# Performance work log

Hardware: AMD Instinct MI355X
Metric: run time of the kernel (lower is better)

The kernel has to match this reference:

```python
import math
import jax, jax.numpy as jnp
import numpy as np

NUM_HEADS = 16
NUM_LANDMARKS = 64
INV_ITERS = 6
ATT_SIZE = 1024
HEAD_SIZE = ATT_SIZE // NUM_HEADS  # dk = 64
NEG = -100000.0


def moore_penrose_pinv(x, num_iter):
    # lucidrains-style iterative Moore-Penrose pseudo-inverse
    abs_x = jnp.abs(x)
    col = abs_x.sum(axis=-1)
    row = abs_x.sum(axis=-2)
    z = jnp.swapaxes(x, -1, -2) / (jnp.max(col) * jnp.max(row))
    I = jnp.eye(x.shape[-1], dtype=x.dtype)
    for _ in range(num_iter):
        xz = x @ z
        z = 0.25 * z @ (13.0 * I - xz @ (15.0 * I - xz @ (7.0 * I - xz)))
    return z


def masked_softmax_scores(k, q, mask):
    # q @ k^T (dk=1: q already scaled) + mask, softmax over last dim
    s = jnp.einsum('bhmd,bhld->bhml', q, k)
    if mask is not None:
        s = s + (1.0 - mask) * NEG
    return jax.nn.softmax(s, axis=-1)


def setup_inputs() -> dict:
    key = jax.random.key(0)
    k1, k2, k3 = jax.random.split(key, 3)
    B, L, D = 4, 4096, 1024
    x = jax.random.normal(k1, (B, L, D), dtype=jnp.float32)
    attention_mask = jnp.ones((B, L), dtype=jnp.float32)
    w_kqv = jax.random.normal(k2, (3 * ATT_SIZE, D), dtype=jnp.float32) * 0.02
    w_out = jax.random.normal(k3, (ATT_SIZE, ATT_SIZE), dtype=jnp.float32) * 0.02
    b_out = jnp.zeros((ATT_SIZE,), dtype=jnp.float32)
    return {"x": x, "attention_mask": attention_mask,
            "w_kqv": w_kqv, "w_out": w_out, "b_out": b_out}


def reference(x, attention_mask, w_kqv, w_out, b_out):
    B, L, D = x.shape
    H, nl, hd = NUM_HEADS, NUM_LANDMARKS, HEAD_SIZE
    seg = L // nl  # landmark segment length (L already a multiple of nl)

    kqv = x @ w_kqv.T  # [B, L, 3A]
    k, q, v = jnp.split(kqv, 3, axis=-1)
    split = lambda t: t.reshape(B, L, H, hd).transpose(0, 2, 1, 3)  # [B,H,L,hd]
    k, q, v = split(k), split(q), split(v)

    mask = attention_mask[:, None, :]  # [B,1,L]
    denom = mask.reshape(B, 1, nl, seg).sum(-1) + 1e-08  # [B,1,nl]
    mask_lm = (denom > 0).astype(x.dtype)  # [B,1,nl]
    denom4 = denom[..., None]              # [B,1,nl,1]
    maskL = mask[..., None]                # [B,1,L,1]

    q = q * maskL
    k = k * maskL
    v = v * maskL

    s1_mask = maskL * mask_lm[..., None, :]               # [B,1,L,nl]
    s2_mask = mask_lm[..., None] * mask_lm[..., None, :]  # [B,1,nl,nl]
    s3_mask = jnp.swapaxes(s1_mask, -1, -2)               # [B,1,nl,L]

    q = q / math.sqrt(HEAD_SIZE)
    q_lm = q.reshape(B, H, nl, seg, hd).sum(-2) / denom4  # [B,H,nl,hd]
    k_lm = k.reshape(B, H, nl, seg, hd).sum(-2) / denom4

    scores_1 = masked_softmax_scores(k_lm, q, s1_mask)     # [B,H,L,nl]
    scores_2 = masked_softmax_scores(k_lm, q_lm, s2_mask)  # [B,H,nl,nl]
    scores_3 = masked_softmax_scores(k, q_lm, s3_mask)     # [B,H,nl,L]

    z_star = moore_penrose_pinv(scores_2, INV_ITERS)       # [B,H,nl,nl]
    out = scores_1 @ (z_star @ (scores_3 @ v))             # [B,H,L,hd]

    out = out.transpose(0, 2, 1, 3).reshape(B, L, H * hd)  # merge heads
    return out @ w_out.T + b_out
```

## Files before the change

### kernel.cpp

```cpp
#include <hip/hip_runtime.h>
#include <hip/hip_bf16.h>


static constexpr int Bn  = 4;
static constexpr int Ln  = 4096;
static constexpr int Dn  = 1024;
static constexpr int Hn  = 16;
static constexpr int HDn = 64;
static constexpr int NLn = 64;
static constexpr int SEGn = 64;
static constexpr int BHn = Bn * Hn;
static constexpr int Mn  = Bn * Ln;
static constexpr int NCH = 8;
#define NEG_BIG (-100000.0f)

static constexpr size_t OFF_KT  = 0;
static constexpr size_t OFF_QT  = 16777216;
static constexpr size_t OFF_VT  = 33554432;
static constexpr size_t OFF_WOH = 33554432;
static constexpr size_t OFF_WH  = 50331648;
static constexpr size_t OFF_QLM = 50331648;
static constexpr size_t OFF_KLM = 50593792;
static constexpr size_t OFF_S2  = 50855936;
static constexpr size_t OFF_Z   = 51118080;
static constexpr size_t OFF_WM  = 51380224;
static constexpr size_t OFF_PM  = 51642368;
static constexpr size_t OFF_PS  = 51675136;
static constexpr size_t OFF_GM  = 51707904;
static constexpr size_t OFF_XS  = 53477376;
static constexpr size_t OFF_PO  = 53477376;

using bf16x8 = __attribute__((ext_vector_type(8))) short;
using f32x16 = __attribute__((ext_vector_type(16))) float;
using s16x4  = __attribute__((ext_vector_type(4))) short;

__device__ __forceinline__ unsigned short f2bf(float f) {
    unsigned int u = __float_as_uint(f);
    return (unsigned short)((u + 0x7fffu + ((u >> 16) & 1u)) >> 16);
}
__device__ __forceinline__ void cvt8r(const float* fs, bf16x8& hv) {
    #pragma unroll
    for (int e = 0; e < 8; ++e) hv[e] = (short)f2bf(fs[e]);
}
typedef __attribute__((address_space(1))) void gvoid;
typedef __attribute__((address_space(3))) void lvoid;
__device__ __forceinline__ void async16(void* l, const void* g) {
    __builtin_amdgcn_global_load_lds((gvoid*)(size_t)g, (lvoid*)l, 16, 0, 0);
}

__global__ __launch_bounds__(256) void k_pack(
    const float* __restrict__ src, unsigned short* __restrict__ dh, int row0)
{
    __shared__ float Ls[128][33];
    const int rt = blockIdx.x, kt = blockIdx.y;
    const int tid = threadIdx.x;
    #pragma unroll
    for (int p = 0; p < 4; ++p) {
        const int row = p * 32 + (tid >> 3);
        const int c4 = (tid & 7) * 4;
        const float4 v = *(const float4*)&src[(size_t)(row0 + rt * 128 + row) * 1024 + kt * 32 + c4];
        Ls[row][c4 + 0] = v.x; Ls[row][c4 + 1] = v.y;
        Ls[row][c4 + 2] = v.z; Ls[row][c4 + 3] = v.w;
    }
    __syncthreads();
    const size_t tb = (size_t)(rt * 32 + kt) * 4096;
    for (int s = tid; s < 512; s += 256) {
        const int g = s >> 7, kk = (s >> 6) & 1, l = s & 63;
        const int row = g * 32 + (l & 31);
        const int k0 = kk * 16 + ((l >> 5) & 1) * 8;
        bf16x8 hv;
        cvt8r(&Ls[row][k0], hv);
        *(bf16x8*)&dh[tb + s * 8] = hv;
    }
}

#define GEMM4W_CORE(A_, B_, NNB)                                               \
    __shared__ __attribute__((aligned(16))) char smem[16384];                  \
    const int tid = threadIdx.x;                                               \
    const int lane = tid & 63, wid = tid >> 6;                                 \
    const int cpx = gridDim.x >> 3;                                            \
    const int wg = (blockIdx.x & 7) * cpx + (blockIdx.x >> 3);                 \
    const int bm = wg / (NNB), bn = wg % (NNB);                                \
    const int wrow = wid >> 1, wcol = wid & 1;                                 \
    const unsigned short* gsrc =                                               \
        (wid < 2 ? (A_) + (size_t)bm * 131072 : (B_) + (size_t)bn * 131072)    \
        + (wid & 1) * 2048 + lane * 8;                                         \
    char* ldst = smem + wid * 4096;                                            \
    f32x16 acc[2][2] = {};                                                     \
    for (int kt = 0; kt < 32; ++kt) {                                          \
        const unsigned short* g = gsrc + (size_t)kt * 4096;                    \
        __syncthreads();                                                       \
        _Pragma("unroll")                                                      \
        for (int i = 0; i < 4; ++i)                                            \
            async16(ldst + i * 1024, g + i * 512);                             \
        __syncthreads();                                                       \
        _Pragma("unroll")                                                      \
        for (int kk = 0; kk < 2; ++kk) {                                       \
            bf16x8 fa[2], fb[2];                                               \
            _Pragma("unroll")                                                  \
            for (int ti = 0; ti < 2; ++ti) {                                   \
                const int o = (((wrow * 2 + ti) * 2 + kk) << 10) + lane * 16;  \
                fa[ti] = *(const bf16x8*)(smem + o);                           \
            }                                                                  \
            _Pragma("unroll")                                                  \
            for (int tj = 0; tj < 2; ++tj) {                                   \
                const int o = (((wcol * 2 + tj) * 2 + kk) << 10) + lane * 16;  \
                fb[tj] = *(const bf16x8*)(smem + 8192 + o);                    \
            }                                                                  \
            _Pragma("unroll")                                                  \
            for (int ti = 0; ti < 2; ++ti)                                     \
                _Pragma("unroll")                                              \
                for (int tj = 0; tj < 2; ++tj)                                 \
                    acc[ti][tj] = __builtin_amdgcn_mfma_f32_32x32x16_bf16(     \
                        fa[ti], fb[tj], acc[ti][tj], 0, 0, 0);                 \
        }                                                                      \
    }

__global__ __launch_bounds__(256) void k_kqv_gemm(
    const unsigned short* __restrict__ xh,
    const unsigned short* __restrict__ wh,
    const float* __restrict__ mask,
    float* __restrict__ Kt, float* __restrict__ Qt, float* __restrict__ Vt,
    int row0)
{
    GEMM4W_CORE(xh, wh, 24)
    const int part = bn >> 3;
    #pragma unroll
    for (int ti = 0; ti < 2; ++ti) {
        #pragma unroll
        for (int tj = 0; tj < 2; ++tj) {
            const int col = (bn * 128 + wcol * 64 + tj * 32 + (lane & 31)) & 1023;
            const int h = col >> 6, d = col & 63;
            #pragma unroll
            for (int r = 0; r < 16; ++r) {
                const int row = row0 + bm * 128 + wrow * 64 + ti * 32
                              + (r & 3) + 8 * (r >> 2) + 4 * (lane >> 5);
                const int b = row >> 12, l = row & 4095;
                const float mk = mask[b * Ln + l];
                const size_t idx = ((size_t)(b * Hn + h) * Ln + l) * HDn + d;
                const float v = acc[ti][tj][r] * mk;
                if (part == 0)      Kt[idx] = v;
                else if (part == 1) Qt[idx] = v * 0.125f;
                else                Vt[idx] = v;
            }
        }
    }
}

__global__ __launch_bounds__(256) void k_out_gemm(
    const unsigned short* __restrict__ ah_,
    const unsigned short* __restrict__ bh_,
    const float* __restrict__ bias, float* __restrict__ out)
{
    GEMM4W_CORE(ah_, bh_, 8)
    #pragma unroll
    for (int ti = 0; ti < 2; ++ti) {
        #pragma unroll
        for (int tj = 0; tj < 2; ++tj) {
            const int col = bn * 128 + wcol * 64 + tj * 32 + (lane & 31);
            const float bb = bias[col];
            #pragma unroll
            for (int r = 0; r < 16; ++r) {
                const int row = bm * 128 + wrow * 64 + ti * 32
                              + (r & 3) + 8 * (r >> 2) + 4 * (lane >> 5);
                out[(size_t)row * Dn + col] = acc[ti][tj][r] + bb;
            }
        }
    }
}

__global__ __launch_bounds__(64) void k_landmarks(
    const float* __restrict__ Kt, const float* __restrict__ Qt,
    const float* __restrict__ mask,
    float* __restrict__ klm, float* __restrict__ qlm, int* __restrict__ gmax)
{
    const int blk = blockIdx.x;
    const int m = blk & 63, bh = blk >> 6, b = bh >> 4;
    const int d = threadIdx.x;
    if (blk == 0 && d < 2) gmax[d] = 0;
    float mv = mask[b * Ln + m * SEGn + d];
    #pragma unroll
    for (int off = 32; off; off >>= 1) mv += __shfl_down(mv, off);
    const float denom = __shfl(mv, 0) + 1e-8f;
    const float* kp = Kt + ((size_t)bh * Ln + m * SEGn) * HDn + d;
    const float* qp = Qt + ((size_t)bh * Ln + m * SEGn) * HDn + d;
    float sk = 0.f, sq = 0.f;
    for (int j = 0; j < SEGn; ++j) {
        sk += kp[(size_t)j * HDn];
        sq += qp[(size_t)j * HDn];
    }
    klm[((size_t)bh * NLn + m) * HDn + d] = sk / denom;
    qlm[((size_t)bh * NLn + m) * HDn + d] = sq / denom;
}

__global__ __launch_bounds__(64) void k_s2(
    const float* __restrict__ qlm, const float* __restrict__ klm,
    float* __restrict__ s2, int* __restrict__ gmax)
{
    const int bh = blockIdx.x;
    __shared__ float ql[64][65];
    __shared__ float kl[64][65];
    __shared__ float sr[64][65];
    const int t = threadIdx.x;
    for (int idx = t; idx < 4096; idx += 64) {
        ql[idx >> 6][idx & 63] = qlm[(size_t)bh * 4096 + idx];
        kl[idx >> 6][idx & 63] = klm[(size_t)bh * 4096 + idx];
    }
    __syncthreads();
    float mx = -1e30f;
    for (int mp = 0; mp < 64; ++mp) {
        float s = 0.f;
        #pragma unroll 8
        for (int d2 = 0; d2 < 64; ++d2) s = fmaf(ql[t][d2], kl[mp][d2], s);
        sr[t][mp] = s;
        mx = fmaxf(mx, s);
    }
    float sum = 0.f;
    for (int mp = 0; mp < 64; ++mp) {
        const float e = expf(sr[t][mp] - mx);
        sr[t][mp] = e;
        sum += e;
    }
    const float inv = 1.f / sum;
    float rs = 0.f;
    for (int mp = 0; mp < 64; ++mp) {
        const float v = sr[t][mp] * inv;
        sr[t][mp] = v;
        s2[(size_t)bh * 4096 + t * 64 + mp] = v;
        rs += fabsf(v);
    }
    __syncthreads();
    float cs = 0.f;
    for (int mm = 0; mm < 64; ++mm) cs += fabsf(sr[mm][t]);
    float rmax = rs, cmax = cs;
    #pragma unroll
    for (int off = 32; off; off >>= 1) {
        rmax = fmaxf(rmax, __shfl_down(rmax, off));
        cmax = fmaxf(cmax, __shfl_down(cmax, off));
    }
    if (t == 0) {
        atomicMax(&gmax[0], __float_as_int(rmax));
        atomicMax(&gmax[1], __float_as_int(cmax));
    }
}

template<int SUB>
__device__ __forceinline__ void mm64v(
    float* C, int ldc, const float* Ag, int lda,
    const float* Bm, int ldb, float dg, float scl)
{
    const int tid = threadIdx.x;
    const int tx = tid & 15, ty = tid >> 4;
    const int i0 = ty << 2, j0 = tx << 2;
    float acc[4][4] = {};
    for (int k0 = 0; k0 < 64; k0 += 4) {
        float4 a4[4], b4[4];
        #pragma unroll
        for (int i = 0; i < 4; ++i)
            a4[i] = *(const float4*)&Ag[(size_t)(i0 + i) * lda + k0];
        #pragma unroll
        for (int kk = 0; kk < 4; ++kk)
            b4[kk] = *(const float4*)&Bm[(size_t)(k0 + kk) * ldb + j0];
        if (SUB) {
            #pragma unroll
            for (int kk = 0; kk < 4; ++kk) {
                float* bp = (float*)&b4[kk];
                #pragma unroll
                for (int j = 0; j < 4; ++j)
                    bp[j] = ((k0 + kk == j0 + j) ? dg : 0.0f) - bp[j];
            }
        }
        #pragma unroll
        for (int i = 0; i < 4; ++i) {
            const float* ap = (const float*)&a4[i];
            #pragma unroll
            for (int kk = 0; kk < 4; ++kk) {
                const float* bp = (const float*)&b4[kk];
                #pragma unroll
                for (int j = 0; j < 4; ++j)
                    acc[i][j] = fmaf(ap[kk], bp[j], acc[i][j]);
            }
        }
    }
    __syncthreads();
    #pragma unroll
    for (int i = 0; i < 4; ++i)
        #pragma unroll
        for (int j = 0; j < 4; ++j) C[(size_t)(i0 + i) * ldc + j0 + j] = scl * acc[i][j];
    __syncthreads();
}

__global__ __launch_bounds__(256) void k_pinv(
    const float* __restrict__ s2, const int* __restrict__ gmax,
    float* __restrict__ zout)
{
    __shared__ float Zb[64][68];
    __shared__ float XZ[64][68];
    __shared__ float Tb[64][68];
    const int bh = blockIdx.x;
    const int tid = threadIdx.x;
    const float* X = s2 + (size_t)bh * 4096;
    const float scale = 1.0f / (__int_as_float(gmax[0]) * __int_as_float(gmax[1]));
    for (int idx = tid; idx < 4096; idx += 256) {
        const int i = idx >> 6, j = idx & 63;
        Zb[i][j] = X[j * 64 + i] * scale;
    }
    __syncthreads();
    for (int it = 0; it < 6; ++it) {
        mm64v<0>(&XZ[0][0], 68, X, 64, &Zb[0][0], 68, 0.f, 1.f);
        mm64v<1>(&Tb[0][0], 68, &XZ[0][0], 68, &XZ[0][0], 68, 7.f, 1.f);
        mm64v<1>(&Tb[0][0], 68, &XZ[0][0], 68, &Tb[0][0], 68, 15.f, 1.f);
        mm64v<1>(&Zb[0][0], 68, &Zb[0][0], 68, &Tb[0][0], 68, 13.f, 0.25f);
    }
    for (int idx = tid; idx < 4096; idx += 256)
        zout[(size_t)bh * 4096 + idx] = Zb[idx >> 6][idx & 63];
}

__global__ __launch_bounds__(256) void k_s3v_part(
    const float* __restrict__ qlm, const float* __restrict__ Kt,
    const float* __restrict__ Vt, const float* __restrict__ mask,
    float* __restrict__ Opart, float* __restrict__ mpart, float* __restrict__ spart)
{
    __shared__ float Sm[64][65];
    __shared__ float Ks[64][65];
    __shared__ float Vs[64][65];
    __shared__ unsigned short Qp[4096];
    __shared__ float red[64][4], red2[64][4];
    __shared__ float rowmax[64], rowsum[64], fac[64], mrow[64];
    const int bh = blockIdx.x, ch = blockIdx.y;
    const int b = bh >> 4;
    const int tid = threadIdx.x;
    const int lane = tid & 63, wid = tid >> 6;
    const int wr = wid >> 1, wc = wid & 1;

    for (int idx = tid; idx < 4096; idx += 256)
        Sm[idx >> 6][idx & 63] = qlm[(size_t)bh * 4096 + idx];
    if (tid < 64) { rowmax[tid] = -1e30f; rowsum[tid] = 0.f; }
    __syncthreads();
    for (int s = tid; s < 512; s += 256) {
        const int g = s >> 8, kc = (s >> 6) & 3, l = s & 63;
        const int row = g * 32 + (l & 31);
        const int k0 = kc * 16 + ((l >> 5) & 1) * 8;
        bf16x8 hv;
        cvt8r(&Sm[row][k0], hv);
        *(bf16x8*)&Qp[s * 8] = hv;
    }
    f32x16 accO = {};
    const int t0beg = ch * (Ln / NCH), t0end = t0beg + (Ln / NCH);
    for (int t0 = t0beg; t0 < t0end; t0 += 64) {
        __syncthreads();
        for (int idx = tid; idx < 4096; idx += 256) {
            const int r = idx >> 6, c2 = idx & 63;
            Ks[r][c2] = Kt[((size_t)bh * Ln + t0 + r) * HDn + c2];
            Vs[r][c2] = Vt[((size_t)bh * Ln + t0 + r) * HDn + c2];
        }
        if (tid < 64) mrow[tid] = mask[b * Ln + t0 + tid];
        __syncthreads();
        f32x16 acc = {};
        #pragma unroll
        for (int kc = 0; kc < 4; ++kc) {
            const bf16x8 a_h = *(const bf16x8*)&Qp[((wr * 4 + kc) * 64 + lane) * 8];
            const int brow = wc * 32 + (lane & 31);
            const int k0 = kc * 16 + (lane >> 5) * 8;
            bf16x8 b_h;
            cvt8r(&Ks[brow][k0], b_h);
            acc = __builtin_amdgcn_mfma_f32_32x32x16_bf16(a_h, b_h, acc, 0, 0, 0);
        }
        #pragma unroll
        for (int r = 0; r < 16; ++r) {
            const int row = wr * 32 + (r & 3) + 8 * (r >> 2) + 4 * (lane >> 5);
            const int col = wc * 32 + (lane & 31);
            Sm[row][col] = acc[r] + (1.f - mrow[col]) * NEG_BIG;
        }
        __syncthreads();
        {
            const int row = tid >> 2, sg = tid & 3, c0 = sg * 16;
            float mx = -1e30f;
            #pragma unroll
            for (int c = 0; c < 16; ++c) mx = fmaxf(mx, Sm[row][c0 + c]);
            red[row][sg] = mx;
            __syncthreads();
            const float nm = fmaxf(rowmax[row],
                fmaxf(fmaxf(red[row][0], red[row][1]), fmaxf(red[row][2], red[row][3])));
            const float f = __expf(rowmax[row] - nm);
            float ps = 0.f;
            #pragma unroll
            for (int c = 0; c < 16; ++c) {
                const float e = __expf(Sm[row][c0 + c] - nm);
                Sm[row][c0 + c] = e;
                ps += e;
            }
            red2[row][sg] = ps;
            __syncthreads();
            if (sg == 0) {
                rowsum[row] = rowsum[row] * f
                    + red2[row][0] + red2[row][1] + red2[row][2] + red2[row][3];
                rowmax[row] = nm;
                fac[row] = f;
            }
        }
        __syncthreads();
        #pragma unroll
        for (int r = 0; r < 16; ++r) {
            const int row = wr * 32 + (r & 3) + 8 * (r >> 2) + 4 * (lane >> 5);
            accO[r] *= fac[row];
        }
        #pragma unroll
        for (int kc = 0; kc < 4; ++kc) {
            const int arow = wr * 32 + (lane & 31);
            const int ak0 = kc * 16 + (lane >> 5) * 8;
            bf16x8 a_h;
            cvt8r(&Sm[arow][ak0], a_h);
            const int bcol = wc * 32 + (lane & 31);
            const int bk0 = kc * 16 + (lane >> 5) * 8;
            float bw[8];
            #pragma unroll
            for (int e = 0; e < 8; ++e) bw[e] = Vs[bk0 + e][bcol];
            bf16x8 b_h;
            cvt8r(bw, b_h);
            accO = __builtin_amdgcn_mfma_f32_32x32x16_bf16(a_h, b_h, accO, 0, 0, 0);
        }
    }
    __syncthreads();
    #pragma unroll
    for (int r = 0; r < 16; ++r) {
        const int row = wr * 32 + (r & 3) + 8 * (r >> 2) + 4 * (lane >> 5);
        Vs[row][wc * 32 + (lane & 31)] = accO[r];
    }
    __syncthreads();
    const size_t ob = (size_t)(bh * NCH + ch) * 4096;
    for (int idx = tid; idx < 4096; idx += 256)
        Opart[ob + idx] = Vs[idx >> 6][idx & 63];
    if (tid < 64) {
        mpart[(bh * NCH + ch) * 64 + tid] = rowmax[tid];
        spart[(bh * NCH + ch) * 64 + tid] = rowsum[tid];
    }
}

__global__ __launch_bounds__(256) void k_mergez(
    const float* __restrict__ Opart, const float* __restrict__ mpart,
    const float* __restrict__ spart, const float* __restrict__ Zs,
    float* __restrict__ Wm)
{
    __shared__ float Sv[64][68];
    __shared__ float Zb[64][68];
    const int bh = blockIdx.x, tid = threadIdx.x;
    for (int idx = tid; idx < 4096; idx += 256)
        Zb[idx >> 6][idx & 63] = Zs[(size_t)bh * 4096 + idx];
    {
        const int r = tid >> 2, c0 = (tid & 3) * 16;
        float e[NCH];
        float M = -1e30f;
        #pragma unroll
        for (int c = 0; c < NCH; ++c) {
            e[c] = mpart[(bh * NCH + c) * 64 + r];
            M = fmaxf(M, e[c]);
        }
        float S = 0.f;
        #pragma unroll
        for (int c = 0; c < NCH; ++c) {
            e[c] = expf(e[c] - M);
            S += spart[(bh * NCH + c) * 64 + r] * e[c];
        }
        const float invS = 1.f / S;
        for (int col = c0; col < c0 + 16; ++col) {
            float o = 0.f;
            #pragma unroll
            for (int c = 0; c < NCH; ++c)
                o += Opart[(size_t)(bh * NCH + c) * 4096 + r * 64 + col] * e[c];
            Sv[r][col] = o * invS;
        }
    }
    __syncthreads();
    const int tx = tid & 15, ty = tid >> 4;
    const int i0 = ty << 2, j0 = tx << 2;
    float acc[4][4] = {};
    for (int k0 = 0; k0 < 64; k0 += 4) {
        float4 a4[4], b4[4];
        #pragma unroll
        for (int i = 0; i < 4; ++i)
            a4[i] = *(const float4*)&Zb[i0 + i][k0];
        #pragma unroll
        for (int kk = 0; kk < 4; ++kk)
            b4[kk] = *(const float4*)&Sv[k0 + kk][j0];
        #pragma unroll
        for (int i = 0; i < 4; ++i) {
            const float* ap = (const float*)&a4[i];
            #pragma unroll
            for (int kk = 0; kk < 4; ++kk) {
                const float* bp = (const float*)&b4[kk];
                #pragma unroll
                for (int j = 0; j < 4; ++j)
                    acc[i][j] = fmaf(ap[kk], bp[j], acc[i][j]);
            }
        }
    }
    #pragma unroll
    for (int i = 0; i < 4; ++i)
        #pragma unroll
        for (int j = 0; j < 4; ++j)
            Wm[(size_t)bh * 4096 + (i0 + i) * 64 + j0 + j] = acc[i][j];
}

__global__ __launch_bounds__(256) void k_attn_out(
    const float* __restrict__ Qt, const float* __restrict__ klm,
    const float* __restrict__ Wm, unsigned short* __restrict__ ah)
{
    const int lt = blockIdx.x;
    const int bh = blockIdx.y;
    const int b = bh >> 4, h = bh & 15;
    __shared__ float Sm[64][65];
    __shared__ float Ks[64][65];
    __shared__ float Ws[64][65];
    __shared__ unsigned short Qp[4096];
    __shared__ float red[64][4], red2[64][4];
    __shared__ float invr[64];
    const int tid = threadIdx.x;
    const int lane = tid & 63, wid = tid >> 6;
    const int wr = wid >> 1, wc = wid & 1;

    for (int idx = tid; idx < 4096; idx += 256) {
        const int r = idx >> 6, c2 = idx & 63;
        Sm[r][c2] = Qt[((size_t)bh * Ln + lt * 64 + r) * HDn + c2];
        Ks[r][c2] = klm[(size_t)bh * 4096 + idx];
        Ws[r][c2] = Wm[(size_t)bh * 4096 + idx];
    }
    __syncthreads();
    for (int s = tid; s < 512; s += 256) {
        const int g = s >> 8, kc = (s >> 6) & 3, l = s & 63;
        const int row = g * 32 + (l & 31);
        const int k0 = kc * 16 + ((l >> 5) & 1) * 8;
        bf16x8 hv;
        cvt8r(&Sm[row][k0], hv);
        *(bf16x8*)&Qp[s * 8] = hv;
    }
    __syncthreads();
    f32x16 acc = {};
    #pragma unroll
    for (int kc = 0; kc < 4; ++kc) {
        const bf16x8 a_h = *(const bf16x8*)&Qp[((wr * 4 + kc) * 64 + lane) * 8];
        const int brow = wc * 32 + (lane & 31);
        const int k0 = kc * 16 + (lane >> 5) * 8;
        bf16x8 b_h;
        cvt8r(&Ks[brow][k0], b_h);
        acc = __builtin_amdgcn_mfma_f32_32x32x16_bf16(a_h, b_h, acc, 0, 0, 0);
    }
    #pragma unroll
    for (int r = 0; r < 16; ++r) {
        const int row = wr * 32 + (r & 3) + 8 * (r >> 2) + 4 * (lane >> 5);
        Sm[row][wc * 32 + (lane & 31)] = acc[r];
    }
    __syncthreads();
    {
        const int row = tid >> 2, sg = tid & 3, c0 = sg * 16;
        float mx = -1e30f;
        #pragma unroll
        for (int c = 0; c < 16; ++c) mx = fmaxf(mx, Sm[row][c0 + c]);
        red[row][sg] = mx;
        __syncthreads();
        mx = fmaxf(fmaxf(red[row][0], red[row][1]), fmaxf(red[row][2], red[row][3]));
        float ps = 0.f;
        #pragma unroll
        for (int c = 0; c < 16; ++c) {
            const float e = __expf(Sm[row][c0 + c] - mx);
            Sm[row][c0 + c] = e;
            ps += e;
        }
        red2[row][sg] = ps;
        __syncthreads();
        if (sg == 0)
            invr[row] = 1.f / (red2[row][0] + red2[row][1] + red2[row][2] + red2[row][3]);
    }
    __syncthreads();
    f32x16 acc2 = {};
    #pragma unroll
    for (int kc = 0; kc < 4; ++kc) {
        const int arow = wr * 32 + (lane & 31);
        const int ak0 = kc * 16 + (lane >> 5) * 8;
        bf16x8 a_h;
        cvt8r(&Sm[arow][ak0], a_h);
        const int bcol = wc * 32 + (lane & 31);
        const int bk0 = kc * 16 + (lane >> 5) * 8;
        float bw[8];
        #pragma unroll
        for (int e = 0; e < 8; ++e) bw[e] = Ws[bk0 + e][bcol];
        bf16x8 b_h;
        cvt8r(bw, b_h);
        acc2 = __builtin_amdgcn_mfma_f32_32x32x16_bf16(a_h, b_h, acc2, 0, 0, 0);
    }
    __syncthreads();
    #pragma unroll
    for (int r = 0; r < 16; ++r) {
        const int row = wr * 32 + (r & 3) + 8 * (r >> 2) + 4 * (lane >> 5);
        Ks[row][wc * 32 + (lane & 31)] = acc2[r];
    }
    __syncthreads();
    const int tx = tid & 15, ty = tid >> 4;
    const int i0 = ty << 2, j0 = tx << 2;
    const int kd = h * 64 + j0;
    const int kt2 = kd >> 5, kc2 = kd & 31;
    const int kk2 = kc2 >> 4, half = (kc2 & 15) >> 3, e0 = kc2 & 7;
    #pragma unroll
    for (int i = 0; i < 4; ++i) {
        const float inv = invr[i0 + i];
        const int gm = b * Ln + lt * 64 + i0 + i;
        const int mt = gm >> 7, g2 = (gm & 127) >> 5, lrow = gm & 31;
        const size_t u = (size_t)(mt * 32 + kt2) * 4096
                       + (size_t)(((g2 * 2 + kk2) * 64 + half * 32 + lrow) * 8 + e0);
        s16x4 hv;
        #pragma unroll
        for (int j = 0; j < 4; ++j)
            hv[j] = (short)f2bf(Ks[i0 + i][j0 + j] * inv);
        *(s16x4*)&ah[u] = hv;
    }
}

extern "C" void kernel_launch(void* const* d_in, const int* in_sizes, int n_in,
                              void* d_out, int out_size, void* d_ws, size_t ws_size,
                              hipStream_t stream)
{
    (void)in_sizes; (void)n_in; (void)out_size;
    const float* x    = (const float*)d_in[0];
    const float* mask = (const float*)d_in[1];
    const float* wkqv = (const float*)d_in[2];
    const float* wout = (const float*)d_in[3];
    const float* bout = (const float*)d_in[4];
    float* out = (float*)d_out;
    float* ws  = (float*)d_ws;

    float* Kt   = ws + OFF_KT;
    float* Qt   = ws + OFF_QT;
    float* Vt   = ws + OFF_VT;
    float* qlm  = ws + OFF_QLM;
    float* klm  = ws + OFF_KLM;
    float* s2   = ws + OFF_S2;
    float* zst  = ws + OFF_Z;
    float* Wm   = ws + OFF_WM;
    int*   gmax = (int*)(ws + OFF_GM);
    float* mpart = ws + OFF_PM;
    float* spart = ws + OFF_PS;
    float* Opart = ws + OFF_PO;
    unsigned short* wh  = (unsigned short*)(ws + OFF_WH);
    unsigned short* woh = (unsigned short*)(ws + OFF_WOH);
    unsigned short* attn_h = (unsigned short*)(ws + OFF_KT);

    int S = 2048;
    if (ws_size >= (size_t)(OFF_XS + 16384 * 512) * 4) S = 16384;
    else if (ws_size >= (size_t)(OFF_XS + 8192 * 512) * 4) S = 8192;
    else if (ws_size >= (size_t)(OFF_XS + 2097152) * 4) S = 4096;
    unsigned short* xhs = (unsigned short*)(ws + OFF_XS);

    k_pack<<<dim3(24, 32), 256, 0, stream>>>(wkqv, wh, 0);
    for (int s = 0; s < Mn / S; ++s) {
        k_pack<<<dim3(S / 128, 32), 256, 0, stream>>>(x, xhs, s * S);
        k_kqv_gemm<<<(S / 128) * 24, 256, 0, stream>>>(
            xhs, wh, mask, Kt, Qt, Vt, s * S);
    }
    k_landmarks<<<BHn * NLn, 64, 0, stream>>>(Kt, Qt, mask, klm, qlm, gmax);
    k_s2<<<BHn, 64, 0, stream>>>(qlm, klm, s2, gmax);
    k_pinv<<<BHn, 256, 0, stream>>>(s2, gmax, zst);
    k_s3v_part<<<dim3(BHn, NCH), 256, 0, stream>>>(qlm, Kt, Vt, mask, Opart, mpart, spart);
    k_pack<<<dim3(8, 32), 256, 0, stream>>>(wout, woh, 0);
    k_mergez<<<BHn, 256, 0, stream>>>(Opart, mpart, spart, zst, Wm);
    k_attn_out<<<dim3(Ln / 64, BHn), 256, 0, stream>>>(Qt, klm, Wm, attn_h);
    k_out_gemm<<<128 * 8, 256, 0, stream>>>(attn_h, woh, bout, out);
}
```

Before: 441.0 us.

## Enlarge GEMM tiles to 256x256 with double-buffered async LDS pipeline

Replaces the 128x128 bf16 MFMA GEMM core with a 256x256 tile where each wave computes a 4x4 grid of 32x32 MFMA tiles. Loads go into two LDS buffers, with the next k-chunk issued asynchronously while the current one is computed and vmcnt waits in place of full syncthreads. The aim is higher arithmetic intensity per loaded byte and hiding global-load latency. The cost is fewer workgroups (256 for the output GEMM), more accumulator registers at occupancy 1, and a remapped XCD-aware block ordering.

After: 527.3 us. +19.6%, slower.

```diff
diff --git a/kernel.cpp b/kernel.cpp
--- a/kernel.cpp
+++ b/kernel.cpp
@@ -74,66 +74,79 @@
     }
 }
 
-#define GEMM4W_CORE(A_, B_, NNB)                                               \
-    __shared__ __attribute__((aligned(16))) char smem[16384];                  \
+#define GEMM256_CORE(A_, B_)                                                   \
+    __shared__ unsigned short smem[2][8192];                                   \
     const int tid = threadIdx.x;                                               \
     const int lane = tid & 63, wid = tid >> 6;                                 \
-    const int cpx = gridDim.x >> 3;                                            \
-    const int wg = (blockIdx.x & 7) * cpx + (blockIdx.x >> 3);                 \
-    const int bm = wg / (NNB), bn = wg % (NNB);                                \
-    const int wrow = wid >> 1, wcol = wid & 1;                                 \
-    const unsigned short* gsrc =                                               \
-        (wid < 2 ? (A_) + (size_t)bm * 131072 : (B_) + (size_t)bn * 131072)    \
-        + (wid & 1) * 2048 + lane * 8;                                         \
-    char* ldst = smem + wid * 4096;                                            \
-    f32x16 acc[2][2] = {};                                                     \
-    for (int kt = 0; kt < 32; ++kt) {                                          \
-        const unsigned short* g = gsrc + (size_t)kt * 4096;                    \
-        __syncthreads();                                                       \
-        _Pragma("unroll")                                                      \
-        for (int i = 0; i < 4; ++i)                                            \
-            async16(ldst + i * 1024, g + i * 512);                             \
-        __syncthreads();                                                       \
-        _Pragma("unroll")                                                      \
-        for (int kk = 0; kk < 2; ++kk) {                                       \
-            bf16x8 fa[2], fb[2];                                               \
+    const int wr = wid >> 1, wc = wid & 1;                                     \
+    const int isB = wid >> 1;                                                  \
+    const int gsel0 = (wid & 1) * 4;                                           \
+    const int dbase = isB * 4096;                                              \
+    const unsigned short* gbase =                                              \
+        (isB ? (B_) + (size_t)bn * 262144 : (A_) + (size_t)bm * 262144)        \
+        + lane * 8;                                                            \
+    const unsigned short* gp[4];                                               \
+    _Pragma("unroll")                                                          \
+    for (int i = 0; i < 4; ++i) {                                              \
+        const int gsel = gsel0 + i;                                            \
+        gp[i] = gbase + (gsel >> 2) * 131072 + (gsel & 3) * 1024;              \
+    }                                                                          \
+    f32x16 acc[4][4] = {};                                                     \
+    {                                                                          \
+        auto ISSUE = [&](int c, int b) {                                       \
+            const size_t so = (size_t)(c >> 1) * 4096 + (size_t)(c & 1) * 512; \
             _Pragma("unroll")                                                  \
-            for (int ti = 0; ti < 2; ++ti) {                                   \
-                const int o = (((wrow * 2 + ti) * 2 + kk) << 10) + lane * 16;  \
-                fa[ti] = *(const bf16x8*)(smem + o);                           \
+            for (int i = 0; i < 4; ++i)                                        \
+                async16(&smem[b][dbase + (gsel0 + i) * 512], gp[i] + so);      \
+        };                                                                     \
+        ISSUE(0, 0);                                                           \
+        ISSUE(1, 1);                                                           \
+        _Pragma("unroll 1")                                                    \
+        for (int c = 0; c < 64; ++c) {                                         \
+            if (c < 63) asm volatile("s_waitcnt vmcnt(4)" ::: "memory");       \
+            else        asm volatile("s_waitcnt vmcnt(0)" ::: "memory");       \
+            __builtin_amdgcn_s_barrier();                                      \
+            __builtin_amdgcn_sched_barrier(0);                                 \
+            const int b = c & 1;                                               \
+            bf16x8 fa[4], fb[4];                                               \
+            _Pragma("unroll")                                                  \
+            for (int t = 0; t < 4; ++t) {                                      \
+                fa[t] = *(const bf16x8*)&smem[b][(wr * 4 + t) * 512 + lane * 8]; \
+                fb[t] = *(const bf16x8*)&smem[b][4096 + (wc * 4 + t) * 512 + lane * 8]; \
             }                                                                  \
             _Pragma("unroll")                                                  \
-            for (int tj = 0; tj < 2; ++tj) {                                   \
-                const int o = (((wcol * 2 + tj) * 2 + kk) << 10) + lane * 16;  \
-                fb[tj] = *(const bf16x8*)(smem + 8192 + o);                    \
-            }                                                                  \
-            _Pragma("unroll")                                                  \
-            for (int ti = 0; ti < 2; ++ti)                                     \
+            for (int ti = 0; ti < 4; ++ti)                                     \
                 _Pragma("unroll")                                              \
-                for (int tj = 0; tj < 2; ++tj)                                 \
+                for (int tj = 0; tj < 4; ++tj)                                 \
                     acc[ti][tj] = __builtin_amdgcn_mfma_f32_32x32x16_bf16(     \
                         fa[ti], fb[tj], acc[ti][tj], 0, 0, 0);                 \
+            __builtin_amdgcn_sched_barrier(0);                                 \
+            if (c + 2 < 64) ISSUE(c + 2, b);                                   \
         }                                                                      \
     }
 
-__global__ __launch_bounds__(256) void k_kqv_gemm(
+__global__ __launch_bounds__(256, 1) void k_kqv_gemm(
     const unsigned short* __restrict__ xh,
     const unsigned short* __restrict__ wh,
     const float* __restrict__ mask,
     float* __restrict__ Kt, float* __restrict__ Qt, float* __restrict__ Vt,
-    int row0)
-{
-    GEMM4W_CORE(xh, wh, 24)
-    const int part = bn >> 3;
-    #pragma unroll
-    for (int ti = 0; ti < 2; ++ti) {
-        #pragma unroll
-        for (int tj = 0; tj < 2; ++tj) {
-            const int col = (bn * 128 + wcol * 64 + tj * 32 + (lane & 31)) & 1023;
-            const int h = col >> 6, d = col & 63;
+    int row0, int nbmx)
+{
+    const int xcd = blockIdx.x & 7;
+    const int q = blockIdx.x >> 3;
+    const int bm = xcd * nbmx + q / 12;
+    const int bn = q % 12;
+    GEMM256_CORE(xh, wh)
+    #pragma unroll
+    for (int ti = 0; ti < 4; ++ti) {
+        #pragma unroll
+        for (int tj = 0; tj < 4; ++tj) {
+            const int col = bn * 256 + wc * 128 + tj * 32 + (lane & 31);
+            const int part = col >> 10, cc = col & 1023;
+            const int h = cc >> 6, d = cc & 63;
             #pragma unroll
             for (int r = 0; r < 16; ++r) {
-                const int row = row0 + bm * 128 + wrow * 64 + ti * 32
+                const int row = row0 + bm * 256 + wr * 128 + ti * 32
                               + (r & 3) + 8 * (r >> 2) + 4 * (lane >> 5);
                 const int b = row >> 12, l = row & 4095;
                 const float mk = mask[b * Ln + l];
@@ -147,21 +160,25 @@
     }
 }
 
-__global__ __launch_bounds__(256) void k_out_gemm(
+__global__ __launch_bounds__(256, 1) void k_out_gemm(
     const unsigned short* __restrict__ ah_,
     const unsigned short* __restrict__ bh_,
     const float* __restrict__ bias, float* __restrict__ out)
 {
-    GEMM4W_CORE(ah_, bh_, 8)
-    #pragma unroll
-    for (int ti = 0; ti < 2; ++ti) {
-        #pragma unroll
-        for (int tj = 0; tj < 2; ++tj) {
-            const int col = bn * 128 + wcol * 64 + tj * 32 + (lane & 31);
+    const int xcd = blockIdx.x & 7;
+    const int q = blockIdx.x >> 3;
+    const int bm = xcd * 8 + (q >> 2);
+    const int bn = q & 3;
+    GEMM256_CORE(ah_, bh_)
+    #pragma unroll
+    for (int ti = 0; ti < 4; ++ti) {
+        #pragma unroll
+        for (int tj = 0; tj < 4; ++tj) {
+            const int col = bn * 256 + wc * 128 + tj * 32 + (lane & 31);
             const float bb = bias[col];
             #pragma unroll
             for (int r = 0; r < 16; ++r) {
-                const int row = bm * 128 + wrow * 64 + ti * 32
+                const int row = bm * 256 + wr * 128 + ti * 32
                               + (r & 3) + 8 * (r >> 2) + 4 * (lane >> 5);
                 out[(size_t)row * Dn + col] = acc[ti][tj][r] + bb;
             }
@@ -649,12 +666,13 @@
     else if (ws_size >= (size_t)(OFF_XS + 8192 * 512) * 4) S = 8192;
     else if (ws_size >= (size_t)(OFF_XS + 2097152) * 4) S = 4096;
     unsigned short* xhs = (unsigned short*)(ws + OFF_XS);
+    const int nbmx = (S / 256) / 8;
 
     k_pack<<<dim3(24, 32), 256, 0, stream>>>(wkqv, wh, 0);
     for (int s = 0; s < Mn / S; ++s) {
         k_pack<<<dim3(S / 128, 32), 256, 0, stream>>>(x, xhs, s * S);
-        k_kqv_gemm<<<(S / 128) * 24, 256, 0, stream>>>(
-            xhs, wh, mask, Kt, Qt, Vt, s * S);
+        k_kqv_gemm<<<(S / 256) * 12, 256, 0, stream>>>(
+            xhs, wh, mask, Kt, Qt, Vt, s * S, nbmx);
     }
     k_landmarks<<<BHn * NLn, 64, 0, stream>>>(Kt, Qt, mask, klm, qlm, gmax);
     k_s2<<<BHn, 64, 0, stream>>>(qlm, klm, s2, gmax);
@@ -663,5 +681,5 @@
     k_pack<<<dim3(8, 32), 256, 0, stream>>>(wout, woh, 0);
     k_mergez<<<BHn, 256, 0, stream>>>(Opart, mpart, spart, zst, Wm);
     k_attn_out<<<dim3(Ln / 64, BHn), 256, 0, stream>>>(Qt, klm, Wm, attn_h);
-    k_out_gemm<<<128 * 8, 256, 0, stream>>>(attn_h, woh, bout, out);
-}
+    k_out_gemm<<<256, 256, 0, stream>>>(attn_h, woh, bout, out);
+}
```

## Merge pinv and s3v partial kernels into one launch to run concurrently

Applied to the files above, without the earlier changes.

Combines the pseudo-inverse kernel and the scores_3·V partial kernel into one launch with an extra grid row. Blocks in that row do the Newton-Schulz iterations while the rest compute the s3v partials. The aim is to overlap the latency-bound 64-block pinv with the independent s3v work and to drop one launch. Shared memory becomes a single union buffer sized for the larger path, which may reduce occupancy for the s3v blocks.

Result: no change. 435.5 us (-1.3%).

```diff
diff --git a/kernel.cpp b/kernel.cpp
--- a/kernel.cpp
+++ b/kernel.cpp
@@ -290,46 +290,51 @@
     __syncthreads();
 }
 
-__global__ __launch_bounds__(256) void k_pinv(
+__global__ __launch_bounds__(256) void k_pinv_s3v(
     const float* __restrict__ s2, const int* __restrict__ gmax,
-    float* __restrict__ zout)
-{
-    __shared__ float Zb[64][68];
-    __shared__ float XZ[64][68];
-    __shared__ float Tb[64][68];
-    const int bh = blockIdx.x;
-    const int tid = threadIdx.x;
-    const float* X = s2 + (size_t)bh * 4096;
-    const float scale = 1.0f / (__int_as_float(gmax[0]) * __int_as_float(gmax[1]));
-    for (int idx = tid; idx < 4096; idx += 256) {
-        const int i = idx >> 6, j = idx & 63;
-        Zb[i][j] = X[j * 64 + i] * scale;
-    }
-    __syncthreads();
-    for (int it = 0; it < 6; ++it) {
-        mm64v<0>(&XZ[0][0], 68, X, 64, &Zb[0][0], 68, 0.f, 1.f);
-        mm64v<1>(&Tb[0][0], 68, &XZ[0][0], 68, &XZ[0][0], 68, 7.f, 1.f);
-        mm64v<1>(&Tb[0][0], 68, &XZ[0][0], 68, &Tb[0][0], 68, 15.f, 1.f);
-        mm64v<1>(&Zb[0][0], 68, &Zb[0][0], 68, &Tb[0][0], 68, 13.f, 0.25f);
-    }
-    for (int idx = tid; idx < 4096; idx += 256)
-        zout[(size_t)bh * 4096 + idx] = Zb[idx >> 6][idx & 63];
-}
-
-__global__ __launch_bounds__(256) void k_s3v_part(
+    float* __restrict__ zout,
     const float* __restrict__ qlm, const float* __restrict__ Kt,
     const float* __restrict__ Vt, const float* __restrict__ mask,
     float* __restrict__ Opart, float* __restrict__ mpart, float* __restrict__ spart)
 {
-    __shared__ float Sm[64][65];
-    __shared__ float Ks[64][65];
-    __shared__ float Vs[64][65];
-    __shared__ unsigned short Qp[4096];
-    __shared__ float red[64][4], red2[64][4];
-    __shared__ float rowmax[64], rowsum[64], fac[64], mrow[64];
+    __shared__ __attribute__((aligned(16))) char shm[61184];
+    const int tid = threadIdx.x;
+
+    if (blockIdx.y == NCH) {
+        float (*Zb)[68] = (float(*)[68])(shm);
+        float (*XZ)[68] = (float(*)[68])(shm + 17408);
+        float (*Tb)[68] = (float(*)[68])(shm + 34816);
+        const int bh = blockIdx.x;
+        const float* X = s2 + (size_t)bh * 4096;
+        const float scale = 1.0f / (__int_as_float(gmax[0]) * __int_as_float(gmax[1]));
+        for (int idx = tid; idx < 4096; idx += 256) {
+            const int i = idx >> 6, j = idx & 63;
+            Zb[i][j] = X[j * 64 + i] * scale;
+        }
+        __syncthreads();
+        for (int it = 0; it < 6; ++it) {
+            mm64v<0>(&XZ[0][0], 68, X, 64, &Zb[0][0], 68, 0.f, 1.f);
+            mm64v<1>(&Tb[0][0], 68, &XZ[0][0], 68, &XZ[0][0], 68, 7.f, 1.f);
+            mm64v<1>(&Tb[0][0], 68, &XZ[0][0], 68, &Tb[0][0], 68, 15.f, 1.f);
+            mm64v<1>(&Zb[0][0], 68, &Zb[0][0], 68, &Tb[0][0], 68, 13.f, 0.25f);
+        }
+        for (int idx = tid; idx < 4096; idx += 256)
+            zout[(size_t)bh * 4096 + idx] = Zb[idx >> 6][idx & 63];
+        return;
+    }
+
+    float (*Sm)[65] = (float(*)[65])(shm);
+    float (*Ks)[65] = (float(*)[65])(shm + 16640);
+    float (*Vs)[65] = (float(*)[65])(shm + 33280);
+    unsigned short* Qp = (unsigned short*)(shm + 49920);
+    float (*red)[4]  = (float(*)[4])(shm + 58112);
+    float (*red2)[4] = (float(*)[4])(shm + 59136);
+    float* rowmax = (float*)(shm + 60160);
+    float* rowsum = (float*)(shm + 60416);
+    float* fac    = (float*)(shm + 60672);
+    float* mrow   = (float*)(shm + 60928);
     const int bh = blockIdx.x, ch = blockIdx.y;
     const int b = bh >> 4;
-    const int tid = threadIdx.x;
     const int lane = tid & 63, wid = tid >> 6;
     const int wr = wid >> 1, wc = wid & 1;
 
@@ -658,8 +663,8 @@
     }
     k_landmarks<<<BHn * NLn, 64, 0, stream>>>(Kt, Qt, mask, klm, qlm, gmax);
     k_s2<<<BHn, 64, 0, stream>>>(qlm, klm, s2, gmax);
-    k_pinv<<<BHn, 256, 0, stream>>>(s2, gmax, zst);
-    k_s3v_part<<<dim3(BHn, NCH), 256, 0, stream>>>(qlm, Kt, Vt, mask, Opart, mpart, spart);
+    k_pinv_s3v<<<dim3(BHn, NCH + 1), 256, 0, stream>>>(
+        s2, gmax, zst, qlm, Kt, Vt, mask, Opart, mpart, spart);
     k_pack<<<dim3(8, 32), 256, 0, stream>>>(wout, woh, 0);
     k_mergez<<<BHn, 256, 0, stream>>>(Opart, mpart, spart, zst, Wm);
     k_attn_out<<<dim3(Ln / 64, BHn), 256, 0, stream>>>(Qt, klm, Wm, attn_h);
```
